# Kernel optimization log

Hardware: AMD Instinct MI355X
Metric: run time of the kernel (lower is better)

The kernel has to match this reference:

```python
import jax, jax.numpy as jnp
import numpy as np

THETA = 10.0      # spike threshold
TAU_SR = 10.0     # synaptic (PSP) alpha-kernel time constant
TAU_REF = 1.0     # refractory alpha-kernel time constant
SCALE_REF = 2.0   # refractory scale (kernel = -scaleRef*theta*(t/tauRef)e^{1-t/tauRef})
TAU_RHO = 1.0     # surrogate-gradient width
SCALE_RHO = 1.0   # surrogate-gradient scale
TS = 1.0          # simulation step (ms)
E = 2.718281828459045

@jax.custom_vjp
def spike_surrogate(u):
    return (u >= THETA).astype(u.dtype)

def _spike_fwd(u):
    return (u >= THETA).astype(u.dtype), u

def _spike_bwd(u, g):
    # SLAYER surrogate spike-pdf gradient
    pdf = (SCALE_RHO / TAU_RHO) * jnp.exp(-jnp.abs(u - THETA) / TAU_RHO)
    return (g * pdf,)

spike_surrogate.defvjp(_spike_fwd, _spike_bwd)

def psp_spike(x):
    # x: (N, ..., T). PSP = causal temporal conv with alpha kernel
    # eps(t) = (t/tauSr) e^{1-t/tauSr}, realized EXACTLY as a 2-state IIR recursion.
    # spike = threshold; each emitted spike injects refractory alpha kernel
    # -scaleRef*theta*(t/tauRef) e^{1-t/tauRef} into the future membrane.
    xt = jnp.moveaxis(x, -1, 0)  # (T, ...)
    a_sr = jnp.exp(jnp.asarray(-TS / TAU_SR, x.dtype))
    a_rf = jnp.exp(jnp.asarray(-TS / TAU_REF, x.dtype))
    c_sr = E / TAU_SR
    c_rf = -SCALE_REF * THETA * E / TAU_REF
    z = jnp.zeros_like(xt[0])
    def step(carry, xi):
        gp, hp, gr, hr = carry
        hp = a_sr * (hp + gp)
        gp = a_sr * gp + xi
        hr = a_rf * (hr + gr)   # same recursion over past spikes
        gr = a_rf * gr
        u = c_sr * hp + c_rf * hr  # membrane = PSP + refractory
        s = spike_surrogate(u)
        return (gp, hp, gr + s, hr), s
    _, st = jax.lax.scan(step, (z, z, z, z), xt)
    return jnp.moveaxis(st, 0, -1)

def sum_pool(x, k):
    # SLAYER pool: conv with constant weight 1.1*theta over kxk window, stride k
    N, C, H, W, T = x.shape
    xs = x.reshape(N, C, H // k, k, W // k, k, T).sum(axis=(3, 5))
    return 1.1 * THETA * xs

def conv2dt(x, w, pad):
    # SLAYER conv = conv3d with kernel (k,k,1): per-time-step 2D conv, T as trailing dim
    return jax.lax.conv_general_dilated(
        x, w[..., None], (1, 1, 1),
        [(pad, pad), (pad, pad), (0, 0)],
        dimension_numbers=('NCHWT', 'OIHWT', 'NCHWT'))

def forward(s_in, w1, w2, w3, w4a, w4b):
    x = psp_spike(sum_pool(s_in, 4))              # (N,2,32,32,T)
    x = psp_spike(conv2dt(x, w1, 2))              # (N,32,32,32,T)
    x = psp_spike(sum_pool(x, 2))                 # (N,32,16,16,T)
    x = psp_spike(conv2dt(x, w2, 1))              # (N,64,16,16,T)
    x = psp_spike(sum_pool(x, 2))                 # (N,64,8,8,T)
    x = psp_spike(conv2dt(x, w3, 1))              # (N,64,8,8,T)
    N, T = x.shape[0], x.shape[-1]
    xf = x.reshape(N, -1, T)                      # (N, 64*8*8, T)
    x = psp_spike(jnp.einsum('nft,of->not', xf, w4a))  # (N,256,T)
    x = psp_spike(jnp.einsum('nct,oc->not', x, w4b))   # (N,11,T)
    return x

def setup_inputs():
    key = jax.random.key(0)
    ks = jax.random.split(key, 6)
    N, T = 4, 300
    # Bernoulli(0.05) event spikes, DVS128 gesture format (N,2,128,128,T)
    s_in = (jax.random.uniform(ks[0], (N, 2, 128, 128, T)) < 0.05).astype(jnp.float32)
    w1 = jax.random.normal(ks[1], (32, 2, 5, 5), jnp.float32) * 10.0 * 0.05   # weightScale=10
    w2 = jax.random.normal(ks[2], (64, 32, 3, 3), jnp.float32) * 20.0 * 0.01  # weightScale=20
    w3 = jax.random.normal(ks[3], (64, 64, 3, 3), jnp.float32) * 20.0 * 0.01  # weightScale=20
    w4a = jax.random.normal(ks[4], (256, 64 * 8 * 8), jnp.float32) * 0.01
    w4b = jax.random.normal(ks[5], (11, 256), jnp.float32) * 0.05
    return {"s_in": s_in, "w1": w1, "w2": w2, "w3": w3, "w4a": w4a, "w4b": w4b}

def reference(s_in, w1, w2, w3, w4a, w4b):
    return forward(s_in, w1, w2, w3, w4a, w4b)
```

## Files before the change

### kernel.cpp

```cpp
#include <hip/hip_runtime.h>
#include <cstdint>

#define TT 300
#define TC 75
#define NBATCH 4

typedef float pf2 __attribute__((ext_vector_type(2)));
typedef _Float16 h8t __attribute__((ext_vector_type(8)));
typedef float f32x4 __attribute__((ext_vector_type(4)));

__device__ __forceinline__ void psp_step(float z, float& gp, float& hp, float& gr, float& hr, float& s_out) {
    hp = 0.90483741803595957f * (hp + gp);
    gp = 0.90483741803595957f * gp + z;
    hr = 0.36787944117144233f * (hr + gr);
    gr = 0.36787944117144233f * gr;
    float u = 0.27182818284590452f * hp + (-54.365636569180904f) * hr;
    float s = (u >= 10.0f) ? 1.0f : 0.0f;
    gr += s;
    s_out = s;
}

template <int R>
__global__ void k_scan_redp(const float* __restrict__ z, float* __restrict__ s,
                            int n_neur, int pstride) {
    int i = blockIdx.x * 64 + threadIdx.x;
    if (i >= n_neur) return;
    const float* zp = z + (size_t)i * TT;
    float* sp = s + (size_t)i * TT;
    float gp = 0.f, hp = 0.f, gr = 0.f, hr = 0.f;
#pragma unroll 1
    for (int c = 0; c < 25; ++c) {
        const float* p = zp + c * 12;
        float4 a0 = *(const float4*)(p);
        float4 a1 = *(const float4*)(p + 4);
        float4 a2 = *(const float4*)(p + 8);
#pragma unroll
        for (int r = 1; r < R; ++r) {
            const float* pr = p + (size_t)r * pstride;
            float4 b0 = *(const float4*)(pr);
            float4 b1 = *(const float4*)(pr + 4);
            float4 b2 = *(const float4*)(pr + 8);
            a0.x += b0.x; a0.y += b0.y; a0.z += b0.z; a0.w += b0.w;
            a1.x += b1.x; a1.y += b1.y; a1.z += b1.z; a1.w += b1.w;
            a2.x += b2.x; a2.y += b2.y; a2.z += b2.z; a2.w += b2.w;
        }
        float4 o0, o1, o2;
        psp_step(a0.x, gp, hp, gr, hr, o0.x);
        psp_step(a0.y, gp, hp, gr, hr, o0.y);
        psp_step(a0.z, gp, hp, gr, hr, o0.z);
        psp_step(a0.w, gp, hp, gr, hr, o0.w);
        psp_step(a1.x, gp, hp, gr, hr, o1.x);
        psp_step(a1.y, gp, hp, gr, hr, o1.y);
        psp_step(a1.z, gp, hp, gr, hr, o1.z);
        psp_step(a1.w, gp, hp, gr, hr, o1.w);
        psp_step(a2.x, gp, hp, gr, hr, o2.x);
        psp_step(a2.y, gp, hp, gr, hr, o2.y);
        psp_step(a2.z, gp, hp, gr, hr, o2.z);
        psp_step(a2.w, gp, hp, gr, hr, o2.w);
        float* q = sp + c * 12;
        *(float4*)(q) = o0;
        *(float4*)(q + 4) = o1;
        *(float4*)(q + 8) = o2;
    }
}

template <int FIN>
__global__ void k_scan_f16(const float* __restrict__ z, _Float16* __restrict__ s16,
                           int n_neur) {
    int i = blockIdx.x * 64 + threadIdx.x;
    if (i >= n_neur) return;
    int n = i / FIN, f = i % FIN;
    const float* zp = z + (size_t)i * TT;
    _Float16* sp = s16 + (size_t)n * TT * FIN + f;
    float gp = 0.f, hp = 0.f, gr = 0.f, hr = 0.f;
#pragma unroll 1
    for (int c = 0; c < 25; ++c) {
        const float* p = zp + c * 12;
        float4 a0 = *(const float4*)(p);
        float4 a1 = *(const float4*)(p + 4);
        float4 a2 = *(const float4*)(p + 8);
        float zv[12] = {a0.x, a0.y, a0.z, a0.w, a1.x, a1.y, a1.z, a1.w, a2.x, a2.y, a2.z, a2.w};
#pragma unroll
        for (int tt = 0; tt < 12; ++tt) {
            float o;
            psp_step(zv[tt], gp, hp, gr, hr, o);
            sp[(size_t)(c * 12 + tt) * FIN] = (_Float16)o;
        }
    }
}

template <int C, int H2, int W2>
__global__ void __launch_bounds__(256) k_spsq_f16(const float* __restrict__ z,
                                                  _Float16* __restrict__ s16) {
    constexpr int H = 2 * H2, W = 2 * W2;
    constexpr int SPB = (C >= 64) ? 1 : 64 / C;
    constexpr int C8 = C / 8;
    __shared__ _Float16 tile[SPB * 12 * C];

    int i = blockIdx.x * 256 + threadIdx.x;
    int q = i & 3;
    int p = i >> 2;
    int c  = p % C;
    int x2 = (p / C) % W2;
    int y2 = (p / (C * W2)) % H2;
    int n  = p / (C * W2 * H2);
    int dy = q >> 1, dx = q & 1;
    const float* zp = z + (((size_t)(n * C + c) * H + 2 * y2 + dy) * W + 2 * x2 + dx) * TT;

    int tid = threadIdx.x;
    int spl = (tid >> 2) / C;

    int wt  = tid % 12;
    int wc8 = (tid / 12) % C8;
    int wsp = tid / (12 * C8);
    bool writer = tid < SPB * 12 * C8;
    int p0 = blockIdx.x * 64;
    int pw = p0 + wsp * C;
    int wx2 = (pw / C) % W2;
    int wy2 = (pw / (C * W2)) % H2;
    int wn  = pw / (C * W2 * H2);
    _Float16* wbase = s16 + ((((size_t)(wn * C8 + wc8) * H2 + wy2) * W2 + wx2) * TT) * 8;

    float gp = 0.f, hp = 0.f, gr = 0.f, hr = 0.f;
    float Gp = 0.f, Hp = 0.f, Gr = 0.f, Hr = 0.f;
#pragma unroll 1
    for (int cc = 0; cc < 25; ++cc) {
        const float* pp = zp + cc * 12;
        float4 a0 = *(const float4*)(pp);
        float4 a1 = *(const float4*)(pp + 4);
        float4 a2 = *(const float4*)(pp + 8);
        float zv[12] = {a0.x, a0.y, a0.z, a0.w, a1.x, a1.y, a1.z, a1.w, a2.x, a2.y, a2.z, a2.w};
        float ov[12];
#pragma unroll
        for (int tt = 0; tt < 12; ++tt) {
            float sq;
            psp_step(zv[tt], gp, hp, gr, hr, sq);
            float t1 = sq + __shfl_xor(sq, 1, 64);
            float pool = t1 + __shfl_xor(t1, 2, 64);
            psp_step(11.0f * pool, Gp, Hp, Gr, Hr, ov[tt]);
        }
        __syncthreads();
        if (q == 0) {
#pragma unroll
            for (int tt = 0; tt < 12; ++tt)
                tile[(spl * 12 + tt) * C + c] = (_Float16)ov[tt];
        }
        __syncthreads();
        if (writer) {
            h8t v;
#pragma unroll
            for (int e = 0; e < 8; ++e) v[e] = tile[(wsp * 12 + wt) * C + wc8 * 8 + e];
            *(h8t*)(wbase + (size_t)(cc * 12 + wt) * 8) = v;
        }
    }
}

__global__ void k_pack_w(const float* __restrict__ w, float* __restrict__ wp, int S, int CO, int total) {
    int i = blockIdx.x * 256 + threadIdx.x;
    if (i >= total) return;
    int co = i % CO, s = i / CO;
    wp[i] = w[co * S + s];
}

__global__ void k_pack_wmfma(const float* __restrict__ w, _Float16* __restrict__ wm,
                             int CIN, int COUT, int total) {
    int i = blockIdx.x * 256 + threadIdx.x;
    if (i >= total) return;
    int lane = i & 63;
    int r = i >> 6;
    int ver = r & 1; r >>= 1;
    int KC = CIN >> 5, CT = COUT >> 4;
    int ct = r % CT; r /= CT;
    int kc = r % KC;
    int tap = r / KC;
    int ky = tap / 3, kx = tap % 3;
    int co  = ct * 16 + (lane & 15);
    int ci0 = kc * 32 + (lane >> 4) * 8;
    _Float16 out[8];
#pragma unroll
    for (int j = 0; j < 8; ++j) {
        float wf = w[((co * CIN + ci0 + j) * 3 + ky) * 3 + kx];
        _Float16 hi = (_Float16)wf;
        out[j] = ver ? (_Float16)((wf - (float)hi) * 4096.0f) : hi;
    }
    *(h8t*)(wm + (size_t)i * 8) = *(h8t*)out;
}

__global__ void k_pack_wfc(const float* __restrict__ w, _Float16* __restrict__ wm,
                           int FIN, int COUT, int total) {
    int i = blockIdx.x * 256 + threadIdx.x;
    if (i >= total) return;
    int lane = i & 63;
    int r = i >> 6;
    int ver = r & 1; r >>= 1;
    int CT = COUT >> 4;
    int ct = r % CT;
    int kg = r / CT;
    int co = ct * 16 + (lane & 15);
    int f0 = kg * 32 + (lane >> 4) * 8;
    _Float16 out[8];
#pragma unroll
    for (int j = 0; j < 8; ++j) {
        float wf = w[(size_t)co * FIN + f0 + j];
        _Float16 hi = (_Float16)wf;
        out[j] = ver ? (_Float16)((wf - (float)hi) * 4096.0f) : hi;
    }
    *(h8t*)(wm + (size_t)i * 8) = *(h8t*)out;
}

__global__ void k_pool4(const float* __restrict__ x, float* __restrict__ z) {
    int idx = blockIdx.x * 256 + threadIdx.x;
    if (idx >= NBATCH * 2 * 32 * 32 * TC) return;
    int tc = idx % TC;
    int p  = idx / TC;
    int w  = p % 32;
    int h  = (p / 32) % 32;
    int nc = p / (32 * 32);
    const float* base = x + (((size_t)nc * 128 + h * 4) * 128 + w * 4) * TT + tc * 4;
    float ax = 0.f, ay = 0.f, az = 0.f, aw = 0.f;
#pragma unroll
    for (int i = 0; i < 4; ++i)
#pragma unroll
        for (int j = 0; j < 4; ++j) {
            float4 v = *(const float4*)(base + ((size_t)i * 128 + j) * TT);
            ax += v.x; ay += v.y; az += v.z; aw += v.w;
        }
    float4 o; o.x = 11.0f * ax; o.y = 11.0f * ay; o.z = 11.0f * az; o.w = 11.0f * aw;
    *(float4*)(z + (size_t)p * TT + tc * 4) = o;
}

template <int SPLIT, int CIN, int COUT, int H, int W, int K, int PAD>
__global__ void __launch_bounds__(256) k_conv_lds(const float* __restrict__ s_in,
                                                  const float* __restrict__ wp,
                                                  float* __restrict__ z) {
    constexpr int CBN = COUT / 16;
    constexpr int CIN_SP = CIN / SPLIT;
    constexpr int S_SP = CIN_SP * K * K;
    __shared__ float wlds[S_SP * COUT];
    int nb8 = gridDim.x >> 3;
    int lb  = (blockIdx.x >> 3) + (blockIdx.x & 7) * nb8;
    int sp = (int)(((size_t)lb * 256) / (CBN * NBATCH * H * W * TC));
    {
        const float4* src = (const float4*)(wp + (size_t)sp * S_SP * COUT);
        float4* dst = (float4*)wlds;
        for (int i = threadIdx.x; i < S_SP * COUT / 4; i += 256) dst[i] = src[i];
    }
    __syncthreads();
    int t = lb * 256 + threadIdx.x;
    int tc = t % TC;     t /= TC;
    int cb = t % CBN;    t /= CBN;
    int x  = t % W;      t /= W;
    int y  = t % H;      t /= H;
    int n  = t % NBATCH;
    const float* sb = s_in + ((size_t)n * CIN + sp * CIN_SP) * H * W * TT + tc * 4;
    pf2 acc[4][4][2];
#pragma unroll
    for (int a = 0; a < 4; ++a)
#pragma unroll
        for (int b = 0; b < 4; ++b)
#pragma unroll
            for (int d = 0; d < 2; ++d) acc[a][b][d] = (pf2){0.f, 0.f};
#pragma unroll 1
    for (int cl = 0; cl < CIN_SP; ++cl) {
#pragma unroll
        for (int ky = 0; ky < K; ++ky) {
            int yy = y + ky - PAD;
            if (yy < 0 || yy >= H) continue;
#pragma unroll
            for (int kx = 0; kx < K; ++kx) {
                int xx = x + kx - PAD;
                if (xx < 0 || xx >= W) continue;
                float4 v = *(const float4*)(sb + ((size_t)(cl * H + yy) * W + xx) * TT);
                pf2 v01 = {v.x, v.y}, v23 = {v.z, v.w};
                const float* wrow = &wlds[((cl * K + ky) * K + kx) * COUT + cb * 16];
#pragma unroll
                for (int cg = 0; cg < 4; ++cg) {
                    float4 wv = *(const float4*)(wrow + cg * 4);
                    float wa[4] = {wv.x, wv.y, wv.z, wv.w};
#pragma unroll
                    for (int c = 0; c < 4; ++c) {
                        pf2 w2 = {wa[c], wa[c]};
                        acc[cg][c][0] = __builtin_elementwise_fma(w2, v01, acc[cg][c][0]);
                        acc[cg][c][1] = __builtin_elementwise_fma(w2, v23, acc[cg][c][1]);
                    }
                }
            }
        }
    }
    float* zb = z + (((size_t)(sp * NBATCH + n) * COUT + cb * 16) * H * W + (size_t)y * W + x) * TT + tc * 4;
#pragma unroll
    for (int cg = 0; cg < 4; ++cg)
#pragma unroll
        for (int c = 0; c < 4; ++c) {
            float4 o;
            o.x = acc[cg][c][0].x; o.y = acc[cg][c][0].y;
            o.z = acc[cg][c][1].x; o.w = acc[cg][c][1].y;
            *(float4*)(zb + (size_t)(cg * 4 + c) * H * W * TT) = o;
        }
}

template <int CIN, int COUT, int H, int W, int YPB>
__global__ void __launch_bounds__(256, 2) k_conv_mfma(const _Float16* __restrict__ s16,
                                                      const _Float16* __restrict__ wm,
                                                      float* __restrict__ z) {
    constexpr int NT = 19;
    constexpr int KC = CIN / 32;
    constexpr int CH = CIN / 8;
    constexpr int XL = W + 2;
    constexpr int CT = COUT / 16;
    constexpr int XPW = W / 4;
    constexpr int ROWS = YPB + 2;
    __shared__ _Float16 lds[ROWS * XL * 16 * CIN];

    int bid = blockIdx.x;
    int tc = bid % NT;
    int yb = ((bid / NT) % (H / YPB)) * YPB;
    int n  = bid / (NT * (H / YPB));
    int tid = threadIdx.x;

    constexpr int TOT = ROWS * XL * CH * 16;
    for (int i = tid; i < TOT; i += 256) {
        int t   = i & 15;
        int c   = (i >> 4) % CH;
        int xc  = ((i >> 4) / CH) % XL;
        int row = ((i >> 4) / CH) / XL;
        int tg = tc * 16 + t;
        int xi = xc - 1;
        int yi = yb + row - 1;
        h8t v;
#pragma unroll
        for (int e = 0; e < 8; ++e) v[e] = (_Float16)0.0f;
        if (xi >= 0 && xi < W && yi >= 0 && yi < H && tg < TT)
            v = *(const h8t*)(s16 + ((((size_t)(n * CH + c) * H + yi) * W + xi) * TT + tg) * 8);
        int swz = (CIN == 32) ? ((t >> 1) & 3) : (t & 7);
        int off = ((row * XL + xc) * 16 + t) * CIN + ((c ^ swz) << 3);
        *(h8t*)(lds + off) = v;
    }
    __syncthreads();

    int lane = tid & 63;
    int wv   = tid >> 6;
    int tl   = lane & 15;
    int hi   = lane >> 4;
    const h8t* wmv = (const h8t*)wm;
    int swz = (CIN == 32) ? ((tl >> 1) & 3) : (tl & 7);
    int tg = tc * 16 + tl;
    bool tv = tg < TT;

#pragma unroll
    for (int yy = 0; yy < YPB; ++yy) {
        f32x4 acc_h[XPW][CT], acc_l[XPW][CT];
#pragma unroll
        for (int a = 0; a < XPW; ++a)
#pragma unroll
            for (int b = 0; b < CT; ++b) {
                acc_h[a][b] = (f32x4){0.f, 0.f, 0.f, 0.f};
                acc_l[a][b] = (f32x4){0.f, 0.f, 0.f, 0.f};
            }
#pragma unroll
        for (int ky = 0; ky < 3; ++ky) {
#pragma unroll
            for (int kx = 0; kx < 3; ++kx) {
                int tap = ky * 3 + kx;
#pragma unroll
                for (int kc = 0; kc < KC; ++kc) {
                    h8t bf[XPW];
#pragma unroll
                    for (int xi = 0; xi < XPW; ++xi) {
                        int x = wv * XPW + xi;
                        int c = kc * 4 + hi;
                        int off = (((yy + ky) * XL + (x + kx)) * 16 + tl) * CIN + ((c ^ swz) << 3);
                        bf[xi] = *(const h8t*)(lds + off);
                    }
#pragma unroll
                    for (int ct = 0; ct < CT; ++ct) {
                        size_t wbase = ((size_t)(tap * KC + kc) * CT + ct) * 2;
                        h8t ah = wmv[(wbase + 0) * 64 + lane];
                        h8t al = wmv[(wbase + 1) * 64 + lane];
#pragma unroll
                        for (int xi = 0; xi < XPW; ++xi) {
                            acc_h[xi][ct] = __builtin_amdgcn_mfma_f32_16x16x32_f16(ah, bf[xi], acc_h[xi][ct], 0, 0, 0);
                            acc_l[xi][ct] = __builtin_amdgcn_mfma_f32_16x16x32_f16(al, bf[xi], acc_l[xi][ct], 0, 0, 0);
                        }
                    }
                }
            }
        }
#pragma unroll
        for (int xi = 0; xi < XPW; ++xi) {
            int x = wv * XPW + xi;
#pragma unroll
            for (int ct = 0; ct < CT; ++ct) {
#pragma unroll
                for (int r = 0; r < 4; ++r) {
                    int co = ct * 16 + hi * 4 + r;
                    if (tv) z[(((size_t)(n * COUT + co) * H + (yb + yy)) * W + x) * TT + tg]
                            = acc_h[xi][ct][r] + acc_l[xi][ct][r] * 2.44140625e-4f;
                }
            }
        }
    }
}

template <int FIN, int OUT>
__global__ void __launch_bounds__(256) k_fc_mfma(const _Float16* __restrict__ s16,
                                                 const _Float16* __restrict__ wm,
                                                 float* __restrict__ z) {
    constexpr int NT = 19;
    constexpr int CT = OUT / 16;
    constexpr int KCH = 512;
    constexpr int NK = FIN / KCH;
    __shared__ _Float16 lds[KCH * 16];

    int bid = blockIdx.x;
    int tc = bid % NT;
    int n  = (bid / NT) % NBATCH;
    int cg = bid / (NT * NBATCH);
    int tid = threadIdx.x;
    int lane = tid & 63, wv = tid >> 6;
    int tl = lane & 15, hi = lane >> 4;
    int ct = cg * 4 + wv;

    f32x4 acc_h = (f32x4){0.f, 0.f, 0.f, 0.f};
    f32x4 acc_l = (f32x4){0.f, 0.f, 0.f, 0.f};
    const h8t* wmv = (const h8t*)wm;

    for (int kb = 0; kb < NK; ++kb) {
        __syncthreads();
#pragma unroll
        for (int j = 0; j < 4; ++j) {
            int chunk = tid + j * 256;
            int c = chunk & 63;
            int t = chunk >> 6;
            int tg = tc * 16 + t;
            h8t v;
#pragma unroll
            for (int e = 0; e < 8; ++e) v[e] = (_Float16)0.0f;
            if (tg < TT) v = *(const h8t*)(s16 + ((size_t)(n * TT + tg) * FIN + kb * KCH + c * 8));
            *(h8t*)(lds + ((t * 64 + (c ^ (t & 7))) << 3)) = v;
        }
        __syncthreads();
#pragma unroll
        for (int kc = 0; kc < KCH / 32; ++kc) {
            int c = kc * 4 + hi;
            h8t bf = *(const h8t*)(lds + ((tl * 64 + (c ^ (tl & 7))) << 3));
            size_t wbase = ((size_t)((kb * (KCH / 32) + kc) * CT + ct)) * 2;
            h8t ah = wmv[(wbase + 0) * 64 + lane];
            h8t al = wmv[(wbase + 1) * 64 + lane];
            acc_h = __builtin_amdgcn_mfma_f32_16x16x32_f16(ah, bf, acc_h, 0, 0, 0);
            acc_l = __builtin_amdgcn_mfma_f32_16x16x32_f16(al, bf, acc_l, 0, 0, 0);
        }
    }
    int tg = tc * 16 + tl;
    if (tg < TT) {
#pragma unroll
        for (int r = 0; r < 4; ++r) {
            int co = ct * 16 + hi * 4 + r;
            z[(size_t)(n * OUT + co) * TT + tg] = acc_h[r] + acc_l[r] * 2.44140625e-4f;
        }
    }
}

template <int OUT, int FIN, int OPER, int FSPLIT>
__global__ void k_fc_a(const float* __restrict__ s, const float* __restrict__ wgt,
                       float* __restrict__ z) {
    constexpr int OG = OUT / OPER, FCH = FIN / FSPLIT;
    int idx = blockIdx.x * 256 + threadIdx.x;
    if (idx >= NBATCH * OG * TC * FSPLIT) return;
    int tc = idx % TC;
    int og = (idx / TC) % OG;
    int n  = (idx / (TC * OG)) % NBATCH;
    int sp = idx / (TC * OG * NBATCH);
    const float* sb = s + (size_t)n * FIN * TT + (size_t)sp * FCH * TT + tc * 4;
    const float* wb = wgt + (size_t)sp * FCH;
    pf2 acc[OPER][2];
#pragma unroll
    for (int k = 0; k < OPER; ++k) { acc[k][0] = (pf2){0.f, 0.f}; acc[k][1] = (pf2){0.f, 0.f}; }
#pragma unroll 2
    for (int f = 0; f < FCH; f += 4) {
        float4 s0 = *(const float4*)(sb + (size_t)(f + 0) * TT);
        float4 s1 = *(const float4*)(sb + (size_t)(f + 1) * TT);
        float4 s2 = *(const float4*)(sb + (size_t)(f + 2) * TT);
        float4 s3 = *(const float4*)(sb + (size_t)(f + 3) * TT);
        pf2 s0a = {s0.x, s0.y}, s0b = {s0.z, s0.w};
        pf2 s1a = {s1.x, s1.y}, s1b = {s1.z, s1.w};
        pf2 s2a = {s2.x, s2.y}, s2b = {s2.z, s2.w};
        pf2 s3a = {s3.x, s3.y}, s3b = {s3.z, s3.w};
#pragma unroll
        for (int k = 0; k < OPER; ++k) {
            float4 wv = *(const float4*)(wb + (size_t)(og * OPER + k) * FIN + f);
            pf2 wx = {wv.x, wv.x}, wy = {wv.y, wv.y}, wz = {wv.z, wv.z}, ww = {wv.w, wv.w};
            pf2 a0 = acc[k][0], a1 = acc[k][1];
            a0 = __builtin_elementwise_fma(wx, s0a, a0);
            a0 = __builtin_elementwise_fma(wy, s1a, a0);
            a0 = __builtin_elementwise_fma(wz, s2a, a0);
            a0 = __builtin_elementwise_fma(ww, s3a, a0);
            a1 = __builtin_elementwise_fma(wx, s0b, a1);
            a1 = __builtin_elementwise_fma(wy, s1b, a1);
            a1 = __builtin_elementwise_fma(wz, s2b, a1);
            a1 = __builtin_elementwise_fma(ww, s3b, a1);
            acc[k][0] = a0; acc[k][1] = a1;
        }
    }
#pragma unroll
    for (int k = 0; k < OPER; ++k) {
        float4 o;
        o.x = acc[k][0].x; o.y = acc[k][0].y; o.z = acc[k][1].x; o.w = acc[k][1].y;
        *(float4*)(z + ((size_t)sp * NBATCH * OUT + (size_t)n * OUT + og * OPER + k) * TT + tc * 4) = o;
    }
}

extern "C" void kernel_launch(void* const* d_in, const int* in_sizes, int n_in,
                              void* d_out, int out_size, void* d_ws, size_t ws_size,
                              hipStream_t stream) {
    const float* s_in = (const float*)d_in[0];
    const float* w1   = (const float*)d_in[1];
    const float* w2   = (const float*)d_in[2];
    const float* w3   = (const float*)d_in[3];
    const float* w4a  = (const float*)d_in[4];
    const float* w4b  = (const float*)d_in[5];
    float* out = (float*)d_out;

    float* Z  = (float*)d_ws;
    float* Sb = Z + 39321600;
    float* WP = Sb + 9830400;
    float* w1p = WP;
    _Float16* wm2 = (_Float16*)(WP + 1600);
    _Float16* wm3 = (_Float16*)(WP + 1600 + 18432);
    _Float16* S16 = (_Float16*)(Z + 25000000);
    _Float16* wm4 = (_Float16*)(Z + 28000000);
    _Float16* s2h = (_Float16*)Sb;
    _Float16* s4h = (_Float16*)(Sb + 5000000);

    auto g = [](int n) { return (n + 255) / 256; };
    auto g64 = [](int n) { return (n + 63) / 64; };

    k_pack_w<<<g(1600), 256, 0, stream>>>(w1, w1p, 50, 32, 1600);
    k_pack_wmfma<<<g(4608), 256, 0, stream>>>(w2, wm2, 32, 64, 4608);
    k_pack_wmfma<<<g(9216), 256, 0, stream>>>(w3, wm3, 64, 64, 9216);

    k_pool4<<<g(614400), 256, 0, stream>>>(s_in, Z);
    k_scan_redp<1><<<g64(8192), 64, 0, stream>>>(Z, Sb, 8192, 0);

    k_conv_lds<1, 2, 32, 32, 32, 5, 2><<<2400, 256, 0, stream>>>(Sb, w1p, Z);
    k_spsq_f16<32, 16, 16><<<512, 256, 0, stream>>>(Z, s2h);

    k_pack_wfc<<<g(262144), 256, 0, stream>>>(w4a, wm4, 4096, 256, 262144);

    k_conv_mfma<32, 64, 16, 16, 2><<<608, 256, 0, stream>>>(s2h, wm2, Z);
    k_spsq_f16<64, 8, 8><<<256, 256, 0, stream>>>(Z, s4h);

    k_conv_mfma<64, 64, 8, 8, 1><<<608, 256, 0, stream>>>(s4h, wm3, Z);
    k_scan_f16<4096><<<g64(16384), 64, 0, stream>>>(Z, S16, 16384);

    k_fc_mfma<4096, 256><<<304, 256, 0, stream>>>(S16, wm4, Z);
    k_scan_redp<1><<<g64(1024), 64, 0, stream>>>(Z, Sb, 1024, 0);

    k_fc_a<11, 256, 1, 1><<<g(3300), 256, 0, stream>>>(Sb, w4b, Z);
    k_scan_redp<1><<<1, 64, 0, stream>>>(Z, out, 44, 0);
}
```

Measured before the change: 638.7 us.

## Fuse layer-1 conv, spike, pool and spike into one MFMA kernel; split conv x

Replaces the FP32 FMA layer-1 5x5 conv and the separate spike/pool/spike kernel with one fused kernel. It runs the conv on f16 MFMA with a hi/lo split of the weights, then does the PSP scan, the 2x2 sum-pool via shuffles and the second PSP scan in-block, writing f16 spikes directly. This removes the large FP32 intermediate Z write and read for layer 1. The later conv_mfma kernels also split the x dimension across blocks, doubling the grid, with launch bounds raised to 4 blocks per SM for occupancy. The cost is that layer 1 now loops serially over 19 time chunks per block, with only 512 blocks.

```diff
diff --git a/kernel.cpp b/kernel.cpp
--- a/kernel.cpp
+++ b/kernel.cpp
@@ -155,13 +155,6 @@
     }
 }
 
-__global__ void k_pack_w(const float* __restrict__ w, float* __restrict__ wp, int S, int CO, int total) {
-    int i = blockIdx.x * 256 + threadIdx.x;
-    if (i >= total) return;
-    int co = i % CO, s = i / CO;
-    wp[i] = w[co * S + s];
-}
-
 __global__ void k_pack_wmfma(const float* __restrict__ w, _Float16* __restrict__ wm,
                              int CIN, int COUT, int total) {
     int i = blockIdx.x * 256 + threadIdx.x;
@@ -208,6 +201,28 @@
     *(h8t*)(wm + (size_t)i * 8) = *(h8t*)out;
 }
 
+__global__ void k_pack_wl1(const float* __restrict__ w, _Float16* __restrict__ wm) {
+    int i = blockIdx.x * 256 + threadIdx.x;
+    if (i >= 768) return;
+    int lane = i & 63;
+    int r = i >> 6;
+    int ver = r & 1;
+    int ch = (r >> 1) & 1;
+    int kc = r >> 2;
+    int co = ch * 16 + (lane & 15);
+    int k0 = kc * 32 + (lane >> 4) * 8;
+    _Float16 out[8];
+#pragma unroll
+    for (int j = 0; j < 8; ++j) {
+        int k = k0 + j;
+        int ky = k >> 4, slot = k & 15, kx = slot >> 1, ci = slot & 1;
+        float wf = (ky < 5 && kx < 5) ? w[((co * 2 + ci) * 5 + ky) * 5 + kx] : 0.f;
+        _Float16 hif = (_Float16)wf;
+        out[j] = ver ? (_Float16)((wf - (float)hif) * 4096.0f) : hif;
+    }
+    *(h8t*)(wm + (size_t)i * 8) = *(h8t*)out;
+}
+
 __global__ void k_pool4(const float* __restrict__ x, float* __restrict__ z) {
     int idx = blockIdx.x * 256 + threadIdx.x;
     if (idx >= NBATCH * 2 * 32 * 32 * TC) return;
@@ -229,93 +244,132 @@
     *(float4*)(z + (size_t)p * TT + tc * 4) = o;
 }
 
-template <int SPLIT, int CIN, int COUT, int H, int W, int K, int PAD>
-__global__ void __launch_bounds__(256) k_conv_lds(const float* __restrict__ s_in,
-                                                  const float* __restrict__ wp,
-                                                  float* __restrict__ z) {
-    constexpr int CBN = COUT / 16;
-    constexpr int CIN_SP = CIN / SPLIT;
-    constexpr int S_SP = CIN_SP * K * K;
-    __shared__ float wlds[S_SP * COUT];
-    int nb8 = gridDim.x >> 3;
-    int lb  = (blockIdx.x >> 3) + (blockIdx.x & 7) * nb8;
-    int sp = (int)(((size_t)lb * 256) / (CBN * NBATCH * H * W * TC));
-    {
-        const float4* src = (const float4*)(wp + (size_t)sp * S_SP * COUT);
-        float4* dst = (float4*)wlds;
-        for (int i = threadIdx.x; i < S_SP * COUT / 4; i += 256) dst[i] = src[i];
-    }
-    __syncthreads();
-    int t = lb * 256 + threadIdx.x;
-    int tc = t % TC;     t /= TC;
-    int cb = t % CBN;    t /= CBN;
-    int x  = t % W;      t /= W;
-    int y  = t % H;      t /= H;
-    int n  = t % NBATCH;
-    const float* sb = s_in + ((size_t)n * CIN + sp * CIN_SP) * H * W * TT + tc * 4;
-    pf2 acc[4][4][2];
-#pragma unroll
-    for (int a = 0; a < 4; ++a)
-#pragma unroll
-        for (int b = 0; b < 4; ++b)
-#pragma unroll
-            for (int d = 0; d < 2; ++d) acc[a][b][d] = (pf2){0.f, 0.f};
+__global__ void __launch_bounds__(256) k_l1_fused(const float* __restrict__ s0,
+                                                  const _Float16* __restrict__ wl1,
+                                                  _Float16* __restrict__ s2h) {
+    constexpr int NT = 19;
+    __shared__ _Float16 stage[7 * 16 * 40];
+    __shared__ float    trans[256 * 17];
+    __shared__ _Float16 tile[4 * 16 * 16];
+
+    int bid = blockIdx.x;
+    int y2 = bid & 15;
+    int xh = (bid >> 4) & 3;
+    int ch = (bid >> 6) & 1;
+    int n  = bid >> 7;
+    int tid = threadIdx.x;
+    int lane = tid & 63;
+    int wv = tid >> 6;
+    int tl = lane & 15;
+    int hi = lane >> 4;
+    int yy = wv >> 1;
+    int xq = wv & 1;
+
+    int q    = tid & 3;
+    int co_s = (tid >> 2) & 15;
+    int x2l_s = tid >> 6;
+    int wt  = tid & 15;
+    int wc8 = (tid >> 4) & 1;
+    int wx  = tid >> 5;
+
+    const h8t* wv4 = (const h8t*)wl1;
+    float gp = 0.f, hp = 0.f, gr = 0.f, hr = 0.f;
+    float Gp = 0.f, Hp = 0.f, Gr = 0.f, Hr = 0.f;
+
 #pragma unroll 1
-    for (int cl = 0; cl < CIN_SP; ++cl) {
-#pragma unroll
-        for (int ky = 0; ky < K; ++ky) {
-            int yy = y + ky - PAD;
-            if (yy < 0 || yy >= H) continue;
-#pragma unroll
-            for (int kx = 0; kx < K; ++kx) {
-                int xx = x + kx - PAD;
-                if (xx < 0 || xx >= W) continue;
-                float4 v = *(const float4*)(sb + ((size_t)(cl * H + yy) * W + xx) * TT);
-                pf2 v01 = {v.x, v.y}, v23 = {v.z, v.w};
-                const float* wrow = &wlds[((cl * K + ky) * K + kx) * COUT + cb * 16];
-#pragma unroll
-                for (int cg = 0; cg < 4; ++cg) {
-                    float4 wv = *(const float4*)(wrow + cg * 4);
-                    float wa[4] = {wv.x, wv.y, wv.z, wv.w};
-#pragma unroll
-                    for (int c = 0; c < 4; ++c) {
-                        pf2 w2 = {wa[c], wa[c]};
-                        acc[cg][c][0] = __builtin_elementwise_fma(w2, v01, acc[cg][c][0]);
-                        acc[cg][c][1] = __builtin_elementwise_fma(w2, v23, acc[cg][c][1]);
-                    }
-                }
+    for (int tc = 0; tc < NT; ++tc) {
+        __syncthreads();
+#pragma unroll
+        for (int ii = 0; ii < 14; ++ii) {
+            int i = tid + ii * 256;
+            int t  = i & 15;
+            int lx = (i >> 4) & 15;
+            int ci = (i >> 8) & 1;
+            int r  = i >> 9;
+            int gx = xh * 8 + lx - 2;
+            int yi = y2 * 2 + r - 2;
+            int tg = tc * 16 + t;
+            float v = 0.f;
+            if (gx >= 0 && gx < 32 && yi >= 0 && yi < 32 && tg < TT)
+                v = s0[(((size_t)(n * 2 + ci) * 32 + yi) * 32 + gx) * TT + tg];
+            stage[(r * 16 + t) * 40 + lx * 2 + ci] = (_Float16)v;
+        }
+        __syncthreads();
+        f32x4 ah4[4], al4[4];
+#pragma unroll
+        for (int xi = 0; xi < 4; ++xi) { ah4[xi] = (f32x4){0.f,0.f,0.f,0.f}; al4[xi] = (f32x4){0.f,0.f,0.f,0.f}; }
+#pragma unroll
+        for (int kc = 0; kc < 3; ++kc) {
+            h8t wa = wv4[((kc * 2 + ch) * 2 + 0) * 64 + lane];
+            h8t wb = wv4[((kc * 2 + ch) * 2 + 1) * 64 + lane];
+            int row = yy + 2 * kc + (hi >> 1);
+#pragma unroll
+            for (int xi = 0; xi < 4; ++xi) {
+                int xo = xq * 4 + xi;
+                const uint32_t* lp = (const uint32_t*)(stage + (row * 16 + tl) * 40 + xo * 2 + (hi & 1) * 8);
+                union { uint32_t u[4]; h8t h; } bu;
+                bu.u[0] = lp[0]; bu.u[1] = lp[1]; bu.u[2] = lp[2]; bu.u[3] = lp[3];
+                ah4[xi] = __builtin_amdgcn_mfma_f32_16x16x32_f16(wa, bu.h, ah4[xi], 0, 0, 0);
+                al4[xi] = __builtin_amdgcn_mfma_f32_16x16x32_f16(wb, bu.h, al4[xi], 0, 0, 0);
             }
         }
-    }
-    float* zb = z + (((size_t)(sp * NBATCH + n) * COUT + cb * 16) * H * W + (size_t)y * W + x) * TT + tc * 4;
-#pragma unroll
-    for (int cg = 0; cg < 4; ++cg)
-#pragma unroll
-        for (int c = 0; c < 4; ++c) {
-            float4 o;
-            o.x = acc[cg][c][0].x; o.y = acc[cg][c][0].y;
-            o.z = acc[cg][c][1].x; o.w = acc[cg][c][1].y;
-            *(float4*)(zb + (size_t)(cg * 4 + c) * H * W * TT) = o;
-        }
-}
-
-template <int CIN, int COUT, int H, int W, int YPB>
-__global__ void __launch_bounds__(256, 2) k_conv_mfma(const _Float16* __restrict__ s16,
+#pragma unroll
+        for (int xi = 0; xi < 4; ++xi) {
+            int xo = xq * 4 + xi;
+#pragma unroll
+            for (int r = 0; r < 4; ++r) {
+                float u = ah4[xi][r] + al4[xi][r] * 2.44140625e-4f;
+                int rowt = ((xo >> 1) * 16 + hi * 4 + r) * 4 + yy * 2 + (xo & 1);
+                trans[rowt * 17 + tl] = u;
+            }
+        }
+        __syncthreads();
+#pragma unroll
+        for (int t = 0; t < 16; ++t) {
+            float u = trans[tid * 17 + t];
+            float sq;
+            psp_step(u, gp, hp, gr, hr, sq);
+            float t1 = sq + __shfl_xor(sq, 1, 64);
+            float pool = t1 + __shfl_xor(t1, 2, 64);
+            float ov;
+            psp_step(11.0f * pool, Gp, Hp, Gr, Hr, ov);
+            if (q == 0) tile[(x2l_s * 16 + t) * 16 + co_s] = (_Float16)ov;
+        }
+        __syncthreads();
+        if (tid < 128) {
+            int tg = tc * 16 + wt;
+            if (tg < TT) {
+                h8t v = *(const h8t*)(tile + (wx * 16 + wt) * 16 + wc8 * 8);
+                int cg8 = ch * 2 + wc8;
+                int x2g = xh * 4 + wx;
+                *(h8t*)(s2h + ((((size_t)(n * 4 + cg8) * 16 + y2) * 16 + x2g) * (size_t)TT + tg) * 8) = v;
+            }
+        }
+    }
+}
+
+template <int CIN, int COUT, int H, int W, int YPB, int XSPL>
+__global__ void __launch_bounds__(256, 4) k_conv_mfma(const _Float16* __restrict__ s16,
                                                       const _Float16* __restrict__ wm,
                                                       float* __restrict__ z) {
     constexpr int NT = 19;
     constexpr int KC = CIN / 32;
     constexpr int CH = CIN / 8;
-    constexpr int XL = W + 2;
+    constexpr int XW = W / XSPL;
+    constexpr int XL = XW + 2;
     constexpr int CT = COUT / 16;
-    constexpr int XPW = W / 4;
+    constexpr int XPW = XW / 4;
     constexpr int ROWS = YPB + 2;
     __shared__ _Float16 lds[ROWS * XL * 16 * CIN];
 
     int bid = blockIdx.x;
     int tc = bid % NT;
-    int yb = ((bid / NT) % (H / YPB)) * YPB;
-    int n  = bid / (NT * (H / YPB));
+    int r0 = bid / NT;
+    int yb = (r0 % (H / YPB)) * YPB;
+    r0 /= (H / YPB);
+    int xh = r0 % XSPL;
+    int n  = r0 / XSPL;
+    int xb = xh * XW;
     int tid = threadIdx.x;
 
     constexpr int TOT = ROWS * XL * CH * 16;
@@ -325,7 +379,7 @@
         int xc  = ((i >> 4) / CH) % XL;
         int row = ((i >> 4) / CH) / XL;
         int tg = tc * 16 + t;
-        int xi = xc - 1;
+        int xi = xb + xc - 1;
         int yi = yb + row - 1;
         h8t v;
 #pragma unroll
@@ -388,7 +442,7 @@
         }
 #pragma unroll
         for (int xi = 0; xi < XPW; ++xi) {
-            int x = wv * XPW + xi;
+            int x = xb + wv * XPW + xi;
 #pragma unroll
             for (int ct = 0; ct < CT; ++ct) {
 #pragma unroll
@@ -524,33 +578,32 @@
     float* Z  = (float*)d_ws;
     float* Sb = Z + 39321600;
     float* WP = Sb + 9830400;
-    float* w1p = WP;
     _Float16* wm2 = (_Float16*)(WP + 1600);
     _Float16* wm3 = (_Float16*)(WP + 1600 + 18432);
     _Float16* S16 = (_Float16*)(Z + 25000000);
     _Float16* wm4 = (_Float16*)(Z + 28000000);
-    _Float16* s2h = (_Float16*)Sb;
+    _Float16* wl1m = (_Float16*)(Z + 30000000);
+    float* s0 = Sb;
+    _Float16* s2h = (_Float16*)(Sb + 2500000);
     _Float16* s4h = (_Float16*)(Sb + 5000000);
 
     auto g = [](int n) { return (n + 255) / 256; };
     auto g64 = [](int n) { return (n + 63) / 64; };
 
-    k_pack_w<<<g(1600), 256, 0, stream>>>(w1, w1p, 50, 32, 1600);
+    k_pack_wl1<<<3, 256, 0, stream>>>(w1, wl1m);
     k_pack_wmfma<<<g(4608), 256, 0, stream>>>(w2, wm2, 32, 64, 4608);
     k_pack_wmfma<<<g(9216), 256, 0, stream>>>(w3, wm3, 64, 64, 9216);
+    k_pack_wfc<<<g(262144), 256, 0, stream>>>(w4a, wm4, 4096, 256, 262144);
 
     k_pool4<<<g(614400), 256, 0, stream>>>(s_in, Z);
-    k_scan_redp<1><<<g64(8192), 64, 0, stream>>>(Z, Sb, 8192, 0);
-
-    k_conv_lds<1, 2, 32, 32, 32, 5, 2><<<2400, 256, 0, stream>>>(Sb, w1p, Z);
-    k_spsq_f16<32, 16, 16><<<512, 256, 0, stream>>>(Z, s2h);
-
-    k_pack_wfc<<<g(262144), 256, 0, stream>>>(w4a, wm4, 4096, 256, 262144);
-
-    k_conv_mfma<32, 64, 16, 16, 2><<<608, 256, 0, stream>>>(s2h, wm2, Z);
+    k_scan_redp<1><<<g64(8192), 64, 0, stream>>>(Z, s0, 8192, 0);
+
+    k_l1_fused<<<512, 256, 0, stream>>>(s0, wl1m, s2h);
+
+    k_conv_mfma<32, 64, 16, 16, 2, 2><<<1216, 256, 0, stream>>>(s2h, wm2, Z);
     k_spsq_f16<64, 8, 8><<<256, 256, 0, stream>>>(Z, s4h);
 
-    k_conv_mfma<64, 64, 8, 8, 1><<<608, 256, 0, stream>>>(s4h, wm3, Z);
+    k_conv_mfma<64, 64, 8, 8, 1, 2><<<1216, 256, 0, stream>>>(s4h, wm3, Z);
     k_scan_f16<4096><<<g64(16384), 64, 0, stream>>>(Z, S16, 16384);
 
     k_fc_mfma<4096, 256><<<304, 256, 0, stream>>>(S16, wm4, Z);
```

Result: slower. 708.0 us (+10.9%).
